# Kernel optimization log

Hardware: AMD Instinct MI355X
Metric: run time of the kernel (lower is better)

## Reference

```python
import jax, jax.numpy as jnp
import numpy as np
import math

EPS = 1e-7
K_NEIGHBORS = 32  # matches init kwarg k

def _project(x, c):
    norm = jnp.linalg.norm(x, axis=-1, keepdims=True).clip(EPS)
    sqrt_c = jnp.sqrt(c).clip(EPS)
    max_norm = (1.0 - EPS) / sqrt_c
    return x * jnp.minimum(max_norm / norm, 1.0)

def _mobius_add(x, y, c):
    x2 = jnp.sum(x * x, axis=-1, keepdims=True)
    y2 = jnp.sum(y * y, axis=-1, keepdims=True)
    xy = jnp.sum(x * y, axis=-1, keepdims=True)
    num = (1 + 2 * c * xy + c * y2) * x + (1 - c * x2) * y
    den = 1 + 2 * c * xy + c * c * x2 * y2
    return _project(num / den.clip(EPS), c)

def _dist(x, y, c):
    sqrt_c = jnp.sqrt(c).clip(EPS)
    diff = _mobius_add(x, -y, c)
    dn = jnp.linalg.norm(diff, axis=-1)
    arg = jnp.minimum(sqrt_c * dn.clip(EPS, 1 - EPS), 1.0 - EPS)
    return 2.0 * jnp.arctanh(arg) / sqrt_c

def _logmap0(y, c):
    sqrt_c = jnp.sqrt(c).clip(EPS)
    yn = jnp.linalg.norm(y, axis=-1, keepdims=True)
    is_zero = yn < EPS
    syn = yn.clip(EPS)
    arg = jnp.minimum(sqrt_c * syn, 1.0 - EPS)
    mag = jnp.arctanh(arg) / sqrt_c
    return jnp.where(is_zero, jnp.zeros_like(y), mag * y / syn)

def _layernorm(x, g, b):
    m = x.mean(-1, keepdims=True)
    v = x.var(-1, keepdims=True)
    return (x - m) / jnp.sqrt(v + 1e-6) * g + b

def setup_inputs() -> dict:
    key = jax.random.key(0)
    B, N, D, P, H = 2, 2048, 512, 3, 8
    ks = jax.random.split(key, 16)
    s = 0.02
    d = {}
    d['x'] = jax.random.normal(ks[0], (B, N, D), dtype=jnp.float32)
    d['positions'] = jax.random.normal(ks[1], (B, N, P), dtype=jnp.float32) * 0.1
    d['c'] = jnp.float32(1.0)
    d['Wq'] = jax.random.normal(ks[2], (D, D), jnp.float32) * s; d['bq'] = jnp.zeros((D,), jnp.float32)
    d['Wk'] = jax.random.normal(ks[3], (D, D), jnp.float32) * s; d['bk'] = jnp.zeros((D,), jnp.float32)
    d['Wv'] = jax.random.normal(ks[4], (D, D), jnp.float32) * s; d['bv'] = jnp.zeros((D,), jnp.float32)
    d['Wg'] = jax.random.normal(ks[5], (P, D), jnp.float32) * s; d['bg'] = jnp.zeros((D,), jnp.float32)
    d['Wo'] = jax.random.normal(ks[6], (D, D), jnp.float32) * s; d['bo'] = jnp.zeros((D,), jnp.float32)
    d['Wf1'] = jax.random.normal(ks[7], (D, 4 * D), jnp.float32) * s; d['bf1'] = jnp.zeros((4 * D,), jnp.float32)
    d['Wf2'] = jax.random.normal(ks[8], (4 * D, D), jnp.float32) * s; d['bf2'] = jnp.zeros((D,), jnp.float32)
    d['g1'] = jnp.ones((D,), jnp.float32); d['b1'] = jnp.zeros((D,), jnp.float32)
    d['g2'] = jnp.ones((D,), jnp.float32); d['b2'] = jnp.zeros((D,), jnp.float32)
    d['ascale'] = jnp.ones((H,), jnp.float32)
    d['fscale'] = jnp.ones((H,), jnp.float32)
    return d

def reference(x, positions, c, Wq, bq, Wk, bk, Wv, bv, Wg, bg, Wo, bo, Wf1, bf1, Wf2, bf2, g1, b1, g2, b2, ascale, fscale):
    B, N, D = x.shape
    H = ascale.shape[0]
    hd = D // H
    K = K_NEIGHBORS

    xn = _layernorm(x, g1, b1)
    q = (xn @ Wq + bq).reshape(B, N, H, hd)
    k = (xn @ Wk + bk).reshape(B, N, H, hd)
    v = (xn @ Wv + bv).reshape(B, N, H, hd)

    # full pairwise hyperbolic distance matrix [B, N, N]
    dmat = _dist(positions[:, :, None, :], positions[:, None, :, :], c)
    idx = jax.lax.top_k(-dmat, K)[1]  # [B, N, K]

    bidx = jnp.arange(B)[:, None, None]
    key_pos = positions[bidx, idx]                 # [B, N, K, P]
    qpos = positions[:, :, None, :]                # [B, N, 1, P]
    geo = _logmap0(_mobius_add(-qpos, key_pos, c), c)
    geo_v = (geo @ Wg + bg).reshape(B, N, K, H, hd)

    kg = k[bidx, idx]                              # [B, N, K, H, hd]
    vg = v[bidx, idx]

    align = jnp.einsum('bnhd,bnkhd->bhnk', q, geo_v)
    feat = jnp.einsum('bnhd,bnkhd->bhnk', q, kg) / math.sqrt(hd)
    scores = fscale[None, :, None, None] * feat + ascale[None, :, None, None] * align
    w = jax.nn.softmax(scores.astype(jnp.float32), axis=-1)
    attn = jnp.einsum('bhnk,bnkhd->bnhd', w, vg).reshape(B, N, D)

    x1 = x + attn @ Wo + bo
    h = _layernorm(x1, g2, b2)
    x2 = x1 + jax.nn.gelu(h @ Wf1 + bf1) @ Wf2 + bf2
    return x2
```

## Files before the change

kernel.cpp:

```cpp
#include <hip/hip_runtime.h>
#include <math.h>

#define EPSF 1e-7f

constexpr int Bb = 2, Nn = 2048, Dd = 512, Hh = 8, HD = 64, KK = 32;
constexpr int ROWS = Bb * Nn;

typedef __attribute__((ext_vector_type(8))) short bf16x8;
typedef __attribute__((ext_vector_type(4))) float f32x4;
typedef __attribute__((ext_vector_type(8))) unsigned short u16x8;
typedef unsigned long long u64;

__device__ inline unsigned short f2bf(float f) {
    union { float f; unsigned int u; } v; v.f = f;
    unsigned int u = v.u;
    unsigned int r = (u + 0x7fffu + ((u >> 16) & 1u)) >> 16;
    return (unsigned short)r;
}

__device__ inline float bf2f(short s) {
    union { unsigned int u; float f; } x;
    x.u = ((unsigned int)(unsigned short)s) << 16;
    return x.f;
}

__device__ inline float gelu_tanh(float v) {
    float u = v + 0.044715f * v * v * v;
    return 0.5f * v * (1.f + tanhf(0.79788456080286535588f * u));
}

__global__ __launch_bounds__(256) void transpose_cvt(const float* __restrict__ in,
                                                     unsigned short* __restrict__ out,
                                                     int K, int N) {
    __shared__ float tile[64][65];
    int k0 = blockIdx.y * 64, n0 = blockIdx.x * 64;
    int t = threadIdx.x;
    int lr = t >> 6, lc = t & 63;
#pragma unroll 4
    for (int p = 0; p < 16; ++p) {
        int r = p * 4 + lr;
        tile[r][lc] = in[(size_t)(k0 + r) * N + n0 + lc];
    }
    __syncthreads();
#pragma unroll 4
    for (int p = 0; p < 16; ++p) {
        int n = p * 4 + lr;
        out[(size_t)(n0 + n) * K + k0 + lc] = f2bf(tile[lc][n]);
    }
}

__global__ __launch_bounds__(256) void transpose_cvt4(const float* __restrict__ w0,
                                                      const float* __restrict__ w1,
                                                      const float* __restrict__ w2,
                                                      const float* __restrict__ w3,
                                                      unsigned short* __restrict__ o0,
                                                      unsigned short* __restrict__ o1,
                                                      unsigned short* __restrict__ o2,
                                                      unsigned short* __restrict__ o3) {
    constexpr int K = 512, N = 512;
    const float* in = (blockIdx.z == 0) ? w0 : (blockIdx.z == 1) ? w1 : (blockIdx.z == 2) ? w2 : w3;
    unsigned short* out = (blockIdx.z == 0) ? o0 : (blockIdx.z == 1) ? o1 : (blockIdx.z == 2) ? o2 : o3;
    __shared__ float tile[64][65];
    int k0 = blockIdx.y * 64, n0 = blockIdx.x * 64;
    int t = threadIdx.x;
    int lr = t >> 6, lc = t & 63;
#pragma unroll 4
    for (int p = 0; p < 16; ++p) {
        int r = p * 4 + lr;
        tile[r][lc] = in[(size_t)(k0 + r) * N + n0 + lc];
    }
    __syncthreads();
#pragma unroll 4
    for (int p = 0; p < 16; ++p) {
        int n = p * 4 + lr;
        out[(size_t)(n0 + n) * K + k0 + lc] = f2bf(tile[lc][n]);
    }
}

__global__ void concat_bias(const float* __restrict__ bq, const float* __restrict__ bk,
                            const float* __restrict__ bv, float* __restrict__ out) {
    int t = blockIdx.x * 256 + threadIdx.x;
    if (t < 512) out[t] = bq[t];
    else if (t < 1024) out[t] = bk[t - 512];
    else if (t < 1536) out[t] = bv[t - 1024];
}

__global__ __launch_bounds__(256) void ln_kernel(const float* __restrict__ x,
                                                 const float* __restrict__ g,
                                                 const float* __restrict__ b,
                                                 unsigned short* __restrict__ out) {
    int row = blockIdx.x * 4 + (threadIdx.x >> 6);
    int lane = threadIdx.x & 63;
    const float* xr = x + (size_t)row * Dd;
    float4 v0 = *(const float4*)(xr + lane * 8);
    float4 v1 = *(const float4*)(xr + lane * 8 + 4);
    float s = v0.x + v0.y + v0.z + v0.w + v1.x + v1.y + v1.z + v1.w;
    float s2 = v0.x * v0.x + v0.y * v0.y + v0.z * v0.z + v0.w * v0.w +
               v1.x * v1.x + v1.y * v1.y + v1.z * v1.z + v1.w * v1.w;
    for (int o = 32; o; o >>= 1) { s += __shfl_xor(s, o); s2 += __shfl_xor(s2, o); }
    float mean = s * (1.f / Dd);
    float var = s2 * (1.f / Dd) - mean * mean;
    float rstd = rsqrtf(var + 1e-6f);
    float4 g0 = *(const float4*)(g + lane * 8);
    float4 g1v = *(const float4*)(g + lane * 8 + 4);
    float4 b0 = *(const float4*)(b + lane * 8);
    float4 b1v = *(const float4*)(b + lane * 8 + 4);
    u16x8 o;
    o[0] = f2bf((v0.x - mean) * rstd * g0.x + b0.x);
    o[1] = f2bf((v0.y - mean) * rstd * g0.y + b0.y);
    o[2] = f2bf((v0.z - mean) * rstd * g0.z + b0.z);
    o[3] = f2bf((v0.w - mean) * rstd * g0.w + b0.w);
    o[4] = f2bf((v1.x - mean) * rstd * g1v.x + b1v.x);
    o[5] = f2bf((v1.y - mean) * rstd * g1v.y + b1v.y);
    o[6] = f2bf((v1.z - mean) * rstd * g1v.z + b1v.z);
    o[7] = f2bf((v1.w - mean) * rstd * g1v.w + b1v.w);
    *(u16x8*)(out + (size_t)row * Dd + lane * 8) = o;
}

template <int EPI, int OBF16>
__global__ __launch_bounds__(256) void gemm64(const unsigned short* __restrict__ A,
                                              const unsigned short* __restrict__ Bt,
                                              const float* __restrict__ bias,
                                              const float* __restrict__ resid,
                                              void* __restrict__ C,
                                              int M, int N, int K, int gridX) {
    __shared__ short As[2][64 * 64];
    __shared__ short Bs[2][64 * 64];
    int nwg = gridDim.x;
    int cpx = nwg >> 3;
    int wgid = blockIdx.x;
    int nid = (wgid & 7) * cpx + (wgid >> 3);
    int bx = nid % gridX, by = nid / gridX;
    int bm = by * 64, bn = bx * 64;
    int tid = threadIdx.x;
    int wave = tid >> 6, lane = tid & 63;
    int wr = wave >> 1, wc = wave & 1;
    f32x4 acc[2][2] = {};

    int srow = wave * 8 + (lane >> 3);
    int scol = (lane & 7) * 8;
    const unsigned short* gA0 = A + (size_t)(bm + srow) * K + scol;
    const unsigned short* gA1 = A + (size_t)(bm + srow + 32) * K + scol;
    const unsigned short* gB0 = Bt + (size_t)(bn + srow) * K + scol;
    const unsigned short* gB1 = Bt + (size_t)(bn + srow + 32) * K + scol;

#define STAGE(buf, kof)                                                                             \
    do {                                                                                            \
        __builtin_amdgcn_global_load_lds((const __attribute__((address_space(1))) void*)(gA0 + (kof)), \
            (__attribute__((address_space(3))) void*)(&As[buf][wave * 512]), 16, 0, 0);             \
        __builtin_amdgcn_global_load_lds((const __attribute__((address_space(1))) void*)(gA1 + (kof)), \
            (__attribute__((address_space(3))) void*)(&As[buf][2048 + wave * 512]), 16, 0, 0);      \
        __builtin_amdgcn_global_load_lds((const __attribute__((address_space(1))) void*)(gB0 + (kof)), \
            (__attribute__((address_space(3))) void*)(&Bs[buf][wave * 512]), 16, 0, 0);             \
        __builtin_amdgcn_global_load_lds((const __attribute__((address_space(1))) void*)(gB1 + (kof)), \
            (__attribute__((address_space(3))) void*)(&Bs[buf][2048 + wave * 512]), 16, 0, 0);      \
    } while (0)

    int nt = K >> 6;
    int cur = 0;
    STAGE(0, 0);
    __syncthreads();
    for (int t = 0; t < nt; ++t) {
        if (t + 1 < nt) STAGE(cur ^ 1, (t + 1) * 64);
        const short* as = &As[cur][0];
        const short* bs = &Bs[cur][0];
#pragma unroll
        for (int kk = 0; kk < 64; kk += 32) {
            int krow = kk + (lane >> 4) * 8;
            bf16x8 a0 = *(const bf16x8*)(as + (wr * 32 + (lane & 15)) * 64 + krow);
            bf16x8 a1 = *(const bf16x8*)(as + (wr * 32 + 16 + (lane & 15)) * 64 + krow);
            bf16x8 b0 = *(const bf16x8*)(bs + (wc * 32 + (lane & 15)) * 64 + krow);
            bf16x8 b1 = *(const bf16x8*)(bs + (wc * 32 + 16 + (lane & 15)) * 64 + krow);
            acc[0][0] = __builtin_amdgcn_mfma_f32_16x16x32_bf16(a0, b0, acc[0][0], 0, 0, 0);
            acc[0][1] = __builtin_amdgcn_mfma_f32_16x16x32_bf16(a0, b1, acc[0][1], 0, 0, 0);
            acc[1][0] = __builtin_amdgcn_mfma_f32_16x16x32_bf16(a1, b0, acc[1][0], 0, 0, 0);
            acc[1][1] = __builtin_amdgcn_mfma_f32_16x16x32_bf16(a1, b1, acc[1][1], 0, 0, 0);
        }
        __syncthreads();
        cur ^= 1;
    }
#undef STAGE

    int cbase = bn + wc * 32 + (lane & 15);
    int rbase = bm + wr * 32 + (lane >> 4) * 4;
    float bias_v[2] = {bias[cbase], bias[cbase + 16]};
#pragma unroll
    for (int mi = 0; mi < 2; ++mi) {
#pragma unroll
        for (int r = 0; r < 4; ++r) {
            int row = rbase + mi * 16 + r;
#pragma unroll
            for (int ni = 0; ni < 2; ++ni) {
                int col = cbase + ni * 16;
                float v = acc[mi][ni][r] + bias_v[ni];
                if (EPI == 1) v += resid[(size_t)row * N + col];
                if (EPI == 2) v = gelu_tanh(v);
                if (OBF16) ((unsigned short*)C)[(size_t)row * N + col] = f2bf(v);
                else ((float*)C)[(size_t)row * N + col] = v;
            }
        }
    }
}

template <int CTRL>
__device__ inline u64 dpp_u64(u64 v) {
    int lo = (int)(unsigned int)v;
    int hi = (int)(unsigned int)(v >> 32);
    lo = __builtin_amdgcn_update_dpp(lo, lo, CTRL, 0xF, 0xF, false);
    hi = __builtin_amdgcn_update_dpp(hi, hi, CTRL, 0xF, 0xF, false);
    return ((u64)(unsigned int)hi << 32) | (unsigned int)lo;
}

__device__ inline u64 wave_min_u64(u64 v) {
    u64 o;
    o = dpp_u64<0xB1>(v);  if (o < v) v = o;
    o = dpp_u64<0x4E>(v);  if (o < v) v = o;
    o = dpp_u64<0x141>(v); if (o < v) v = o;
    o = dpp_u64<0x140>(v); if (o < v) v = o;
    o = __shfl_xor(v, 16); if (o < v) v = o;
    o = __shfl_xor(v, 32); if (o < v) v = o;
    return v;
}

__global__ __launch_bounds__(256, 3) void topk_kernel(const float* __restrict__ pos,
                                                      const float* __restrict__ cp,
                                                      int* __restrict__ idx_out) {
    __shared__ float s_px[Nn], s_py[Nn], s_pz[Nn], s_u[Nn];
    __shared__ int s_out[4][KK];
    int b = blockIdx.x >> 9;
    int q0 = (blockIdx.x & 511) * 4;
    int t = threadIdx.x;
    float c = *cp;
    const float* pb = pos + (size_t)b * Nn * 3;
    for (int j = t; j < Nn; j += 256) {
        float px = pb[j * 3 + 0], py = pb[j * 3 + 1], pz = pb[j * 3 + 2];
        s_px[j] = px; s_py[j] = py; s_pz[j] = pz;
        s_u[j] = c * (px * px + py * py + pz * pz);
    }
    __syncthreads();
    int wave = t >> 6, lane = t & 63;
    int n = q0 + wave;
    float qx = s_px[n], qy = s_py[n], qz = s_pz[n];
    float cx2 = s_u[n];
    float x2 = cx2 / c;
    float B = 1.f - cx2;
    float rc = 1.f / c;
    float B2rc = B * B * rc;
    float m2c = -2.f * c;
    float m2B = -2.f * B;
    float key[32];
#pragma unroll
    for (int i = 0; i < 32; ++i) {
        int j = i * 64 + lane;
        float dot = qx * s_px[j] + qy * s_py[j] + qz * s_pz[j];
        float su = s_u[j];
        float r = fmaf(m2c, dot, 1.f);
        float A = r + su;
        float den = fmaf(cx2, su, r);
        float p1 = x2 * A;
        float q1 = A * dot;
        float t1 = fmaf(m2B, q1, B2rc * su);
        float num2 = fmaf(p1, A, t1);
        float rd = __builtin_amdgcn_rcpf(den);
        key[i] = num2 * rd * rd;
    }
    const u64 MAXK = ~0ull;
    u64 B0 = MAXK, B1 = MAXK, B2 = MAXK, B3 = MAXK;
#pragma unroll
    for (int i = 0; i < 32; ++i) {
        u64 k = ((u64)__float_as_uint(key[i]) << 32) | (unsigned int)(i * 64 + lane);
        if (k < B3) {
            B3 = k;
            if (B3 < B2) { u64 tmp = B2; B2 = B3; B3 = tmp; }
            if (B2 < B1) { u64 tmp = B1; B1 = B2; B2 = tmp; }
            if (B1 < B0) { u64 tmp = B0; B0 = B1; B1 = tmp; }
        }
    }
    int bcount = 4, consumed = 0;
    u64 last = 0;
    for (int s2 = 0; s2 < KK; ++s2) {
        bool need = (bcount == 0) && (consumed < 32);
        if (__any(need)) {
            if (need) {
                B0 = MAXK; B1 = MAXK; B2 = MAXK; B3 = MAXK;
#pragma unroll
                for (int i = 0; i < 32; ++i) {
                    u64 k = ((u64)__float_as_uint(key[i]) << 32) | (unsigned int)(i * 64 + lane);
                    if (k > last && k < B3) {
                        B3 = k;
                        if (B3 < B2) { u64 tmp = B2; B2 = B3; B3 = tmp; }
                        if (B2 < B1) { u64 tmp = B1; B1 = B2; B2 = tmp; }
                        if (B1 < B0) { u64 tmp = B0; B0 = B1; B1 = tmp; }
                    }
                }
                int rem = 32 - consumed;
                bcount = rem < 4 ? rem : 4;
            }
        }
        u64 offer = (bcount > 0) ? B0 : MAXK;
        u64 g = wave_min_u64(offer);
        if (lane == 0) s_out[wave][s2] = (int)(unsigned int)g;
        if (offer == g) {
            B0 = B1; B1 = B2; B2 = B3; B3 = MAXK;
            --bcount; ++consumed; last = g;
        }
    }
    if (lane < KK) idx_out[(size_t)(b * Nn + n) * KK + lane] = s_out[wave][lane];
}

__global__ __launch_bounds__(256) void attn_kernel(const unsigned short* __restrict__ qkv,
                                                   const int* __restrict__ idx,
                                                   const float* __restrict__ pos,
                                                   const float* __restrict__ Wg,
                                                   const float* __restrict__ bg,
                                                   const float* __restrict__ ascale,
                                                   const float* __restrict__ fscale,
                                                   const float* __restrict__ cp,
                                                   unsigned short* __restrict__ out) {
    constexpr int QS = 1536;
    int bid = blockIdx.x;
    int xcd = bid & 7, slot = bid >> 3;
    int b = xcd >> 2;
    int n = (xcd & 3) * 512 + slot;
    int bn = b * Nn + n;
    int t = threadIdx.x;
    int wave = t >> 6, lane = t & 63;
    __shared__ float s_q[Dd];
    __shared__ float s_geo[KK][3];
    __shared__ int s_idx[KK];
    __shared__ float s_qg[Hh][3];
    __shared__ float s_qb[Hh];
    __shared__ float s_dot[KK][9];
    __shared__ float s_w[Hh][KK];
    __shared__ float s_part[4][Dd];
    float c = *cp;
    if (t >= 64 && t < 96) s_idx[t - 64] = idx[(size_t)bn * KK + (t - 64)];
    if (t < 64) {
        bf16x8 q8 = *(const bf16x8*)(qkv + (size_t)bn * QS + t * 8);
#pragma unroll
        for (int j = 0; j < 8; ++j) s_q[t * 8 + j] = bf2f(q8[j]);
    }
    __syncthreads();
    if (t < KK) {
        const float* qp = pos + (size_t)bn * 3;
        const float* kp = pos + (size_t)(b * Nn + s_idx[t]) * 3;
        float xx = -qp[0], xyc = -qp[1], xz = -qp[2];
        float yx = kp[0], yy = kp[1], yz = kp[2];
        float x2 = xx * xx + xyc * xyc + xz * xz;
        float y2 = yx * yx + yy * yy + yz * yz;
        float xy = xx * yx + xyc * yy + xz * yz;
        float Av = 1.f + 2.f * c * xy + c * y2;
        float Bv = 1.f - c * x2;
        float den = fmaxf(1.f + 2.f * c * xy + c * c * x2 * y2, EPSF);
        float mx = (Av * xx + Bv * yx) / den;
        float my = (Av * xyc + Bv * yy) / den;
        float mz = (Av * xz + Bv * yz) / den;
        float rn = fmaxf(sqrtf(mx * mx + my * my + mz * mz), EPSF);
        float sqrt_c = fmaxf(sqrtf(c), EPSF);
        float max_norm = (1.f - EPSF) / sqrt_c;
        float scpr = fminf(max_norm / rn, 1.f);
        mx *= scpr; my *= scpr; mz *= scpr;
        float yn = sqrtf(mx * mx + my * my + mz * mz);
        if (yn < EPSF) {
            s_geo[t][0] = 0.f; s_geo[t][1] = 0.f; s_geo[t][2] = 0.f;
        } else {
            float syn = fmaxf(yn, EPSF);
            float arg = fminf(sqrt_c * syn, 1.f - EPSF);
            float mag = atanhf(arg) / sqrt_c;
            float f = mag / syn;
            s_geo[t][0] = mx * f; s_geo[t][1] = my * f; s_geo[t][2] = mz * f;
        }
    } else if (t >= 64 && t < 88) {
        int h = (t - 64) / 3, p = (t - 64) % 3;
        float acc = 0.f;
        for (int d2 = 0; d2 < HD; ++d2) acc += s_q[h * HD + d2] * Wg[p * Dd + h * HD + d2];
        s_qg[h][p] = acc;
    } else if (t >= 96 && t < 104) {
        int h = t - 96;
        float acc = 0.f;
        for (int d2 = 0; d2 < HD; ++d2) acc += s_q[h * HD + d2] * bg[h * HD + d2];
        s_qb[h] = acc;
    }
    {
#pragma unroll
        for (int r = 0; r < 8; ++r) {
            int kk = wave * 8 + r;
            int nk = s_idx[kk];
            bf16x8 k8 = *(const bf16x8*)(qkv + (size_t)(b * Nn + nk) * QS + 512 + lane * 8);
            float p = 0.f;
#pragma unroll
            for (int j = 0; j < 8; ++j) p = fmaf(bf2f(k8[j]), s_q[lane * 8 + j], p);
            p += __shfl_xor(p, 1);
            p += __shfl_xor(p, 2);
            p += __shfl_xor(p, 4);
            if ((lane & 7) == 0) s_dot[kk][lane >> 3] = p;
        }
    }
    __syncthreads();
    {
        int h = t >> 5, kk = t & 31;
        float align = s_geo[kk][0] * s_qg[h][0] + s_geo[kk][1] * s_qg[h][1] +
                      s_geo[kk][2] * s_qg[h][2] + s_qb[h];
        float scv = fscale[h] * s_dot[kk][h] * 0.125f + ascale[h] * align;
        float m = scv;
        for (int o = 16; o; o >>= 1) m = fmaxf(m, __shfl_xor(m, o));
        float e = expf(scv - m);
        float ss = e;
        for (int o = 16; o; o >>= 1) ss += __shfl_xor(ss, o);
        s_w[h][kk] = e / ss;
    }
    __syncthreads();
    {
        float acc[8] = {0.f, 0.f, 0.f, 0.f, 0.f, 0.f, 0.f, 0.f};
        int h = lane >> 3;
#pragma unroll
        for (int r = 0; r < 8; ++r) {
            int kk = wave * 8 + r;
            int nk = s_idx[kk];
            bf16x8 v8 = *(const bf16x8*)(qkv + (size_t)(b * Nn + nk) * QS + 1024 + lane * 8);
            float wgt = s_w[h][kk];
#pragma unroll
            for (int j = 0; j < 8; ++j) acc[j] = fmaf(bf2f(v8[j]), wgt, acc[j]);
        }
#pragma unroll
        for (int j = 0; j < 8; ++j) s_part[wave][lane * 8 + j] = acc[j];
    }
    __syncthreads();
    for (int d = t; d < Dd; d += 256) {
        float s = s_part[0][d] + s_part[1][d] + s_part[2][d] + s_part[3][d];
        out[(size_t)bn * Dd + d] = f2bf(s);
    }
}

extern "C" void kernel_launch(void* const* d_in, const int* in_sizes, int n_in,
                              void* d_out, int out_size, void* d_ws, size_t ws_size,
                              hipStream_t stream) {
    const float* x   = (const float*)d_in[0];
    const float* pos = (const float*)d_in[1];
    const float* cp  = (const float*)d_in[2];
    const float* Wq  = (const float*)d_in[3];
    const float* bq  = (const float*)d_in[4];
    const float* Wk  = (const float*)d_in[5];
    const float* bk  = (const float*)d_in[6];
    const float* Wv  = (const float*)d_in[7];
    const float* bv  = (const float*)d_in[8];
    const float* Wg  = (const float*)d_in[9];
    const float* bg  = (const float*)d_in[10];
    const float* Wo  = (const float*)d_in[11];
    const float* bo  = (const float*)d_in[12];
    const float* Wf1 = (const float*)d_in[13];
    const float* bf1 = (const float*)d_in[14];
    const float* Wf2 = (const float*)d_in[15];
    const float* bf2 = (const float*)d_in[16];
    const float* g1  = (const float*)d_in[17];
    const float* b1  = (const float*)d_in[18];
    const float* g2  = (const float*)d_in[19];
    const float* b2  = (const float*)d_in[20];
    const float* asc = (const float*)d_in[21];
    const float* fsc = (const float*)d_in[22];
    float* out = (float*)d_out;
    char* ws = (char*)d_ws;

    unsigned short* qkv_bf  = (unsigned short*)(ws + 0);
    unsigned short* t_bf    = (unsigned short*)(ws + 0);
    unsigned short* xn_bf   = (unsigned short*)(ws + 25165824);
    float*          x1      = (float*)(ws + 29360128);
    unsigned short* attn_bf = (unsigned short*)(ws + 37748736);
    unsigned short* wqkv_t  = (unsigned short*)(ws + 41943040);
    unsigned short* wo_t    = (unsigned short*)(ws + 43515904);
    unsigned short* wf1_t   = (unsigned short*)(ws + 44040192);
    unsigned short* wf2_t   = (unsigned short*)(ws + 46137344);
    int*            idx     = (int*)(ws + 48234496);
    float*          bqkv    = (float*)(ws + 48758784);

    transpose_cvt4<<<dim3(8, 8, 4), 256, 0, stream>>>(Wq, Wk, Wv, Wo,
        wqkv_t, wqkv_t + 512 * 512, wqkv_t + 1024 * 512, wo_t);
    transpose_cvt<<<dim3(32, 8), 256, 0, stream>>>(Wf1, wf1_t, 512, 2048);
    transpose_cvt<<<dim3(8, 32), 256, 0, stream>>>(Wf2, wf2_t, 2048, 512);
    concat_bias<<<6, 256, 0, stream>>>(bq, bk, bv, bqkv);

    ln_kernel<<<ROWS / 4, 256, 0, stream>>>(x, g1, b1, xn_bf);
    gemm64<0, 1><<<1536, 256, 0, stream>>>(xn_bf, wqkv_t, bqkv, nullptr, qkv_bf, ROWS, 1536, 512, 24);
    topk_kernel<<<ROWS / 4, 256, 0, stream>>>(pos, cp, idx);
    attn_kernel<<<ROWS, 256, 0, stream>>>(qkv_bf, idx, pos, Wg, bg, asc, fsc, cp, attn_bf);
    gemm64<1, 0><<<512, 256, 0, stream>>>(attn_bf, wo_t, bo, x, x1, ROWS, 512, 512, 8);
    ln_kernel<<<ROWS / 4, 256, 0, stream>>>(x1, g2, b2, xn_bf);
    gemm64<2, 1><<<2048, 256, 0, stream>>>(xn_bf, wf1_t, bf1, nullptr, t_bf, ROWS, 2048, 512, 32);
    gemm64<1, 0><<<512, 256, 0, stream>>>(t_bf, wf2_t, bf2, x1, out, ROWS, 512, 2048, 8);
}
```

Baseline: 157.2 us.

## Merge prep kernels, co-launch QKV GEMM with top-k, swizzle GEMM LDS

Combines the weight transposes, bias concat and first layernorm into one launch. The QKV GEMM and the top-k neighbour search now share a single launch via block-index dispatch, so the two independent stages can overlap. Separately, it XOR-swizzles the GEMM's LDS column layout to reduce bank conflicts on the MFMA operand loads. The merged kernels lose the topk kernel's occupancy hint and force the larger shared allocation onto every block, which may lower occupancy.

```diff
diff --git a/kernel.cpp b/kernel.cpp
--- a/kernel.cpp
+++ b/kernel.cpp
@@ -29,11 +29,10 @@
     return 0.5f * v * (1.f + tanhf(0.79788456080286535588f * u));
 }
 
-__global__ __launch_bounds__(256) void transpose_cvt(const float* __restrict__ in,
-                                                     unsigned short* __restrict__ out,
-                                                     int K, int N) {
-    __shared__ float tile[64][65];
-    int k0 = blockIdx.y * 64, n0 = blockIdx.x * 64;
+__device__ __forceinline__ void tcvt(float (*tile)[65], const float* __restrict__ in,
+                                     unsigned short* __restrict__ out,
+                                     int K, int N, int bx, int by) {
+    int k0 = by * 64, n0 = bx * 64;
     int t = threadIdx.x;
     int lr = t >> 6, lc = t & 63;
 #pragma unroll 4
@@ -49,48 +48,11 @@
     }
 }
 
-__global__ __launch_bounds__(256) void transpose_cvt4(const float* __restrict__ w0,
-                                                      const float* __restrict__ w1,
-                                                      const float* __restrict__ w2,
-                                                      const float* __restrict__ w3,
-                                                      unsigned short* __restrict__ o0,
-                                                      unsigned short* __restrict__ o1,
-                                                      unsigned short* __restrict__ o2,
-                                                      unsigned short* __restrict__ o3) {
-    constexpr int K = 512, N = 512;
-    const float* in = (blockIdx.z == 0) ? w0 : (blockIdx.z == 1) ? w1 : (blockIdx.z == 2) ? w2 : w3;
-    unsigned short* out = (blockIdx.z == 0) ? o0 : (blockIdx.z == 1) ? o1 : (blockIdx.z == 2) ? o2 : o3;
-    __shared__ float tile[64][65];
-    int k0 = blockIdx.y * 64, n0 = blockIdx.x * 64;
-    int t = threadIdx.x;
-    int lr = t >> 6, lc = t & 63;
-#pragma unroll 4
-    for (int p = 0; p < 16; ++p) {
-        int r = p * 4 + lr;
-        tile[r][lc] = in[(size_t)(k0 + r) * N + n0 + lc];
-    }
-    __syncthreads();
-#pragma unroll 4
-    for (int p = 0; p < 16; ++p) {
-        int n = p * 4 + lr;
-        out[(size_t)(n0 + n) * K + k0 + lc] = f2bf(tile[lc][n]);
-    }
-}
-
-__global__ void concat_bias(const float* __restrict__ bq, const float* __restrict__ bk,
-                            const float* __restrict__ bv, float* __restrict__ out) {
-    int t = blockIdx.x * 256 + threadIdx.x;
-    if (t < 512) out[t] = bq[t];
-    else if (t < 1024) out[t] = bk[t - 512];
-    else if (t < 1536) out[t] = bv[t - 1024];
-}
-
-__global__ __launch_bounds__(256) void ln_kernel(const float* __restrict__ x,
-                                                 const float* __restrict__ g,
-                                                 const float* __restrict__ b,
-                                                 unsigned short* __restrict__ out) {
-    int row = blockIdx.x * 4 + (threadIdx.x >> 6);
-    int lane = threadIdx.x & 63;
+__device__ __forceinline__ void ln_row(const float* __restrict__ x,
+                                       const float* __restrict__ g,
+                                       const float* __restrict__ b,
+                                       unsigned short* __restrict__ out,
+                                       int row, int lane) {
     const float* xr = x + (size_t)row * Dd;
     float4 v0 = *(const float4*)(xr + lane * 8);
     float4 v1 = *(const float4*)(xr + lane * 8 + 4);
@@ -117,18 +79,55 @@
     *(u16x8*)(out + (size_t)row * Dd + lane * 8) = o;
 }
 
+__global__ __launch_bounds__(256) void ln_kernel(const float* __restrict__ x,
+                                                 const float* __restrict__ g,
+                                                 const float* __restrict__ b,
+                                                 unsigned short* __restrict__ out) {
+    ln_row(x, g, b, out, blockIdx.x * 4 + (threadIdx.x >> 6), threadIdx.x & 63);
+}
+
+__global__ __launch_bounds__(256) void prep_kernel(
+    const float* __restrict__ Wq, const float* __restrict__ Wk,
+    const float* __restrict__ Wv, const float* __restrict__ Wo,
+    const float* __restrict__ Wf1, const float* __restrict__ Wf2,
+    const float* __restrict__ bq, const float* __restrict__ bk, const float* __restrict__ bv,
+    const float* __restrict__ x, const float* __restrict__ g1, const float* __restrict__ b1,
+    unsigned short* __restrict__ wqkv_t, unsigned short* __restrict__ wo_t,
+    unsigned short* __restrict__ wf1_t, unsigned short* __restrict__ wf2_t,
+    float* __restrict__ bqkv, unsigned short* __restrict__ xn) {
+    __shared__ float tile[64][65];
+    int bid = blockIdx.x;
+    if (bid < 256) {
+        int z = bid >> 6, r = bid & 63;
+        const float* in = (z == 0) ? Wq : (z == 1) ? Wk : (z == 2) ? Wv : Wo;
+        unsigned short* out = (z == 0) ? wqkv_t : (z == 1) ? wqkv_t + 262144
+                            : (z == 2) ? wqkv_t + 524288 : wo_t;
+        tcvt(tile, in, out, 512, 512, r & 7, r >> 3);
+    } else if (bid < 512) {
+        int r = bid - 256;
+        tcvt(tile, Wf1, wf1_t, 512, 2048, r & 31, r >> 5);
+    } else if (bid < 768) {
+        int r = bid - 512;
+        tcvt(tile, Wf2, wf2_t, 2048, 512, r & 7, r >> 3);
+    } else if (bid < 774) {
+        int t = (bid - 768) * 256 + threadIdx.x;
+        if (t < 512) bqkv[t] = bq[t];
+        else if (t < 1024) bqkv[t] = bk[t - 512];
+        else if (t < 1536) bqkv[t] = bv[t - 1024];
+    } else {
+        ln_row(x, g1, b1, xn, (bid - 774) * 4 + (threadIdx.x >> 6), threadIdx.x & 63);
+    }
+}
+
 template <int EPI, int OBF16>
-__global__ __launch_bounds__(256) void gemm64(const unsigned short* __restrict__ A,
-                                              const unsigned short* __restrict__ Bt,
-                                              const float* __restrict__ bias,
-                                              const float* __restrict__ resid,
-                                              void* __restrict__ C,
-                                              int M, int N, int K, int gridX) {
-    __shared__ short As[2][64 * 64];
-    __shared__ short Bs[2][64 * 64];
-    int nwg = gridDim.x;
+__device__ __forceinline__ void gemm64_body(short* __restrict__ As, short* __restrict__ Bs,
+                                            const unsigned short* __restrict__ A,
+                                            const unsigned short* __restrict__ Bt,
+                                            const float* __restrict__ bias,
+                                            const float* __restrict__ resid,
+                                            void* __restrict__ C,
+                                            int N, int K, int gridX, int nwg, int wgid) {
     int cpx = nwg >> 3;
-    int wgid = blockIdx.x;
     int nid = (wgid & 7) * cpx + (wgid >> 3);
     int bx = nid % gridX, by = nid / gridX;
     int bm = by * 64, bn = bx * 64;
@@ -138,22 +137,22 @@
     f32x4 acc[2][2] = {};
 
     int srow = wave * 8 + (lane >> 3);
-    int scol = (lane & 7) * 8;
+    int scol = ((lane & 7) ^ (lane >> 3)) * 8;
     const unsigned short* gA0 = A + (size_t)(bm + srow) * K + scol;
     const unsigned short* gA1 = A + (size_t)(bm + srow + 32) * K + scol;
     const unsigned short* gB0 = Bt + (size_t)(bn + srow) * K + scol;
     const unsigned short* gB1 = Bt + (size_t)(bn + srow + 32) * K + scol;
 
-#define STAGE(buf, kof)                                                                             \
-    do {                                                                                            \
+#define STAGE(buf, kof)                                                                                 \
+    do {                                                                                                \
         __builtin_amdgcn_global_load_lds((const __attribute__((address_space(1))) void*)(gA0 + (kof)), \
-            (__attribute__((address_space(3))) void*)(&As[buf][wave * 512]), 16, 0, 0);             \
+            (__attribute__((address_space(3))) void*)(As + (buf) * 4096 + wave * 512), 16, 0, 0);       \
         __builtin_amdgcn_global_load_lds((const __attribute__((address_space(1))) void*)(gA1 + (kof)), \
-            (__attribute__((address_space(3))) void*)(&As[buf][2048 + wave * 512]), 16, 0, 0);      \
+            (__attribute__((address_space(3))) void*)(As + (buf) * 4096 + 2048 + wave * 512), 16, 0, 0);\
         __builtin_amdgcn_global_load_lds((const __attribute__((address_space(1))) void*)(gB0 + (kof)), \
-            (__attribute__((address_space(3))) void*)(&Bs[buf][wave * 512]), 16, 0, 0);             \
+            (__attribute__((address_space(3))) void*)(Bs + (buf) * 4096 + wave * 512), 16, 0, 0);       \
         __builtin_amdgcn_global_load_lds((const __attribute__((address_space(1))) void*)(gB1 + (kof)), \
-            (__attribute__((address_space(3))) void*)(&Bs[buf][2048 + wave * 512]), 16, 0, 0);      \
+            (__attribute__((address_space(3))) void*)(Bs + (buf) * 4096 + 2048 + wave * 512), 16, 0, 0);\
     } while (0)
 
     int nt = K >> 6;
@@ -162,15 +161,15 @@
     __syncthreads();
     for (int t = 0; t < nt; ++t) {
         if (t + 1 < nt) STAGE(cur ^ 1, (t + 1) * 64);
-        const short* as = &As[cur][0];
-        const short* bs = &Bs[cur][0];
+        const short* as = As + cur * 4096;
+        const short* bs = Bs + cur * 4096;
 #pragma unroll
         for (int kk = 0; kk < 64; kk += 32) {
-            int krow = kk + (lane >> 4) * 8;
-            bf16x8 a0 = *(const bf16x8*)(as + (wr * 32 + (lane & 15)) * 64 + krow);
-            bf16x8 a1 = *(const bf16x8*)(as + (wr * 32 + 16 + (lane & 15)) * 64 + krow);
-            bf16x8 b0 = *(const bf16x8*)(bs + (wc * 32 + (lane & 15)) * 64 + krow);
-            bf16x8 b1 = *(const bf16x8*)(bs + (wc * 32 + 16 + (lane & 15)) * 64 + krow);
+            int kx = (kk + (lane >> 4) * 8) ^ ((lane & 7) << 3);
+            bf16x8 a0 = *(const bf16x8*)(as + (wr * 32 + (lane & 15)) * 64 + kx);
+            bf16x8 a1 = *(const bf16x8*)(as + (wr * 32 + 16 + (lane & 15)) * 64 + kx);
+            bf16x8 b0 = *(const bf16x8*)(bs + (wc * 32 + (lane & 15)) * 64 + kx);
+            bf16x8 b1 = *(const bf16x8*)(bs + (wc * 32 + 16 + (lane & 15)) * 64 + kx);
             acc[0][0] = __builtin_amdgcn_mfma_f32_16x16x32_bf16(a0, b0, acc[0][0], 0, 0, 0);
             acc[0][1] = __builtin_amdgcn_mfma_f32_16x16x32_bf16(a0, b1, acc[0][1], 0, 0, 0);
             acc[1][0] = __builtin_amdgcn_mfma_f32_16x16x32_bf16(a1, b0, acc[1][0], 0, 0, 0);
@@ -200,6 +199,18 @@
             }
         }
     }
+}
+
+template <int EPI, int OBF16>
+__global__ __launch_bounds__(256) void gemm64(const unsigned short* __restrict__ A,
+                                              const unsigned short* __restrict__ Bt,
+                                              const float* __restrict__ bias,
+                                              const float* __restrict__ resid,
+                                              void* __restrict__ C,
+                                              int N, int K, int gridX) {
+    __shared__ short As[2 * 64 * 64];
+    __shared__ short Bs[2 * 64 * 64];
+    gemm64_body<EPI, OBF16>(As, Bs, A, Bt, bias, resid, C, N, K, gridX, gridDim.x, blockIdx.x);
 }
 
 template <int CTRL>
@@ -222,13 +233,16 @@
     return v;
 }
 
-__global__ __launch_bounds__(256, 3) void topk_kernel(const float* __restrict__ pos,
-                                                      const float* __restrict__ cp,
-                                                      int* __restrict__ idx_out) {
-    __shared__ float s_px[Nn], s_py[Nn], s_pz[Nn], s_u[Nn];
-    __shared__ int s_out[4][KK];
-    int b = blockIdx.x >> 9;
-    int q0 = (blockIdx.x & 511) * 4;
+__device__ __forceinline__ void topk_body(char* smem, const float* __restrict__ pos,
+                                          const float* __restrict__ cp,
+                                          int* __restrict__ idx_out, int bid) {
+    float* s_px = (float*)smem;
+    float* s_py = s_px + Nn;
+    float* s_pz = s_py + Nn;
+    float* s_u  = s_pz + Nn;
+    int* s_out  = (int*)(s_u + Nn);
+    int b = bid >> 9;
+    int q0 = (bid & 511) * 4;
     int t = threadIdx.x;
     float c = *cp;
     const float* pb = pos + (size_t)b * Nn * 3;
@@ -299,13 +313,30 @@
         }
         u64 offer = (bcount > 0) ? B0 : MAXK;
         u64 g = wave_min_u64(offer);
-        if (lane == 0) s_out[wave][s2] = (int)(unsigned int)g;
+        if (lane == 0) s_out[wave * KK + s2] = (int)(unsigned int)g;
         if (offer == g) {
             B0 = B1; B1 = B2; B2 = B3; B3 = MAXK;
             --bcount; ++consumed; last = g;
         }
     }
-    if (lane < KK) idx_out[(size_t)(b * Nn + n) * KK + lane] = s_out[wave][lane];
+    if (lane < KK) idx_out[(size_t)(b * Nn + n) * KK + lane] = s_out[wave * KK + lane];
+}
+
+__global__ __launch_bounds__(256) void qkv_topk_kernel(const unsigned short* __restrict__ A,
+                                                       const unsigned short* __restrict__ Wqkv,
+                                                       const float* __restrict__ bqkv,
+                                                       unsigned short* __restrict__ qkv,
+                                                       const float* __restrict__ pos,
+                                                       const float* __restrict__ cp,
+                                                       int* __restrict__ idx_out) {
+    __shared__ __align__(16) char smem[33280];
+    if (blockIdx.x < 1536) {
+        short* As = (short*)smem;
+        short* Bs = (short*)(smem + 16384);
+        gemm64_body<0, 1>(As, Bs, A, Wqkv, bqkv, nullptr, qkv, 1536, 512, 24, 1536, blockIdx.x);
+    } else {
+        topk_body(smem, pos, cp, idx_out, blockIdx.x - 1536);
+    }
 }
 
 __global__ __launch_bounds__(256) void attn_kernel(const unsigned short* __restrict__ qkv,
@@ -473,18 +504,12 @@
     int*            idx     = (int*)(ws + 48234496);
     float*          bqkv    = (float*)(ws + 48758784);
 
-    transpose_cvt4<<<dim3(8, 8, 4), 256, 0, stream>>>(Wq, Wk, Wv, Wo,
-        wqkv_t, wqkv_t + 512 * 512, wqkv_t + 1024 * 512, wo_t);
-    transpose_cvt<<<dim3(32, 8), 256, 0, stream>>>(Wf1, wf1_t, 512, 2048);
-    transpose_cvt<<<dim3(8, 32), 256, 0, stream>>>(Wf2, wf2_t, 2048, 512);
-    concat_bias<<<6, 256, 0, stream>>>(bq, bk, bv, bqkv);
-
-    ln_kernel<<<ROWS / 4, 256, 0, stream>>>(x, g1, b1, xn_bf);
-    gemm64<0, 1><<<1536, 256, 0, stream>>>(xn_bf, wqkv_t, bqkv, nullptr, qkv_bf, ROWS, 1536, 512, 24);
-    topk_kernel<<<ROWS / 4, 256, 0, stream>>>(pos, cp, idx);
+    prep_kernel<<<1798, 256, 0, stream>>>(Wq, Wk, Wv, Wo, Wf1, Wf2, bq, bk, bv,
+                                          x, g1, b1, wqkv_t, wo_t, wf1_t, wf2_t, bqkv, xn_bf);
+    qkv_topk_kernel<<<2560, 256, 0, stream>>>(xn_bf, wqkv_t, bqkv, qkv_bf, pos, cp, idx);
     attn_kernel<<<ROWS, 256, 0, stream>>>(qkv_bf, idx, pos, Wg, bg, asc, fsc, cp, attn_bf);
-    gemm64<1, 0><<<512, 256, 0, stream>>>(attn_bf, wo_t, bo, x, x1, ROWS, 512, 512, 8);
+    gemm64<1, 0><<<512, 256, 0, stream>>>(attn_bf, wo_t, bo, x, x1, 512, 512, 8);
     ln_kernel<<<ROWS / 4, 256, 0, stream>>>(x1, g2, b2, xn_bf);
-    gemm64<2, 1><<<2048, 256, 0, stream>>>(xn_bf, wf1_t, bf1, nullptr, t_bf, ROWS, 2048, 512, 32);
-    gemm64<1, 0><<<512, 256, 0, stream>>>(t_bf, wf2_t, bf2, x1, out, ROWS, 512, 2048, 8);
-}
+    gemm64<2, 1><<<2048, 256, 0, stream>>>(xn_bf, wf1_t, bf1, nullptr, t_bf, 2048, 512, 32);
+    gemm64<1, 0><<<512, 256, 0, stream>>>(t_bf, wf2_t, bf2, x1, out, 512, 2048, 8);
+}
```

After: 138.3 us. -12.0%, faster.
